# Kernel tuning notes

Measured on AMD Instinct MI355X. Metric: run time of the kernel, lower is better.

## Reference

```python
import jax, jax.numpy as jnp
import numpy as np
from jax import lax

EPS = 1e-5

def conv2d(x, w, b=None, pad=1):
    # x: [N,C,H,W], w: [O,I,kh,kw]
    out = lax.conv_general_dilated(x, w, window_strides=(1, 1),
                                   padding=[(pad, pad), (pad, pad)],
                                   dimension_numbers=('NCHW', 'OIHW', 'NCHW'))
    if b is not None:
        out = out + b[None, :, None, None]
    return out

def batchnorm(x, gamma, beta):
    # training-mode BN (biased batch stats), matching torch default train()
    mean = jnp.mean(x, axis=(0, 2, 3), keepdims=True)
    var = jnp.var(x, axis=(0, 2, 3), keepdims=True)
    xn = (x - mean) * lax.rsqrt(var + EPS)
    return xn * gamma[None, :, None, None] + beta[None, :, None, None]

def setup_inputs() -> dict:
    key = jax.random.key(0)
    ks = jax.random.split(key, 16)
    B, Cin, H, W = 4, 3, 256, 256
    Cout = 128
    NP = 32
    npat = NP // 3  # 10 per normal region
    qc_in = Cout + 3 * npat + NP  # 190 (actual concat width)

    def kaiming(k, shape, fan_in):
        return jax.random.normal(k, shape, jnp.float32) * np.sqrt(2.0 / fan_in)

    inp = {
        'x': jax.random.normal(ks[0], (B, Cin, H, W), jnp.float32),
        'conv1_w': kaiming(ks[1], (Cout // 2, Cin, 3, 3), Cin * 9),
        'conv1_b': jnp.zeros((Cout // 2,), jnp.float32),
        'bn1_g': jnp.ones((Cout // 2,), jnp.float32),
        'bn1_b': jnp.zeros((Cout // 2,), jnp.float32),
        'conv2_w': kaiming(ks[2], (Cout, Cout // 2, 3, 3), (Cout // 2) * 9),
        'conv2_b': jnp.zeros((Cout,), jnp.float32),
        'bn2_g': jnp.ones((Cout,), jnp.float32),
        'bn2_b': jnp.zeros((Cout,), jnp.float32),
        'core_p': jax.random.normal(ks[3], (npat, Cout, 3, 3), jnp.float32),
        'clad_p': jax.random.normal(ks[4], (npat, Cout, 3, 3), jnp.float32),
        'ferr_p': jax.random.normal(ks[5], (npat, Cout, 3, 3), jnp.float32),
        'anom_p': jax.random.normal(ks[6], (NP, Cout, 3, 3), jnp.float32),
        'qa1_w': kaiming(ks[7], (64, qc_in, 1, 1), qc_in),
        'qa1_b': jnp.zeros((64,), jnp.float32),
        'qa2_w': kaiming(ks[8], (1, 64, 1, 1), 64),
        'qa2_b': jnp.zeros((1,), jnp.float32),
        'cls_w': kaiming(ks[9], (4, qc_in, 1, 1), qc_in),
        'cls_b': jnp.zeros((4,), jnp.float32),
    }
    return inp

def reference(x, conv1_w, conv1_b, bn1_g, bn1_b, conv2_w, conv2_b, bn2_g, bn2_b,
              core_p, clad_p, ferr_p, anom_p, qa1_w, qa1_b, qa2_w, qa2_b, cls_w, cls_b):
    # feature extractor: conv-bn-relu x2
    h = jax.nn.relu(batchnorm(conv2d(x, conv1_w, conv1_b), bn1_g, bn1_b))
    features = jax.nn.relu(batchnorm(conv2d(h, conv2_w, conv2_b), bn2_g, bn2_b))

    # pattern matching: the per-pattern loop of 1-out-channel convs + sigmoid
    # is exactly one multi-output-channel conv (no bias) + sigmoid
    normal_w = jnp.concatenate([core_p, clad_p, ferr_p], axis=0)  # [30,C,3,3]
    all_matches = jax.nn.sigmoid(conv2d(features, normal_w))       # [B,30,H,W]
    anomaly_matches = jax.nn.sigmoid(conv2d(features, anom_p))     # [B,32,H,W]

    quality_input = jnp.concatenate([features, all_matches, anomaly_matches], axis=1)
    q = jax.nn.relu(conv2d(quality_input, qa1_w, qa1_b, pad=0))
    quality_scores = jax.nn.sigmoid(conv2d(q, qa2_w, qa2_b, pad=0))

    classifications = conv2d(quality_input, cls_w, cls_b, pad=0)
    region_logits = classifications[:, :3]
    anomaly_logits = classifications[:, 3:4]
    region_probs = jax.nn.softmax(region_logits, axis=1)
    anomaly_probs = jax.nn.sigmoid(anomaly_logits)

    return (features, region_logits, anomaly_logits, all_matches,
            anomaly_matches, quality_scores, region_probs, anomaly_probs)
```

## Files before the change

### kernel.cpp

```cpp
#include <hip/hip_runtime.h>
#include <hip/hip_bf16.h>

typedef unsigned short u16;
typedef __attribute__((ext_vector_type(8)))  short s8v;
typedef __attribute__((ext_vector_type(4)))  short s4v;
typedef __attribute__((ext_vector_type(16))) float f16v;

#define HWX 65536
#define EPSV 1e-5f

#define O0 0u
#define O1 33554432u
#define O2 34340864u
#define O3 34603008u
#define O4 42467328u
#define O5 50855936u
#define O6 51118080u
#define O7 51904512u

__device__ __forceinline__ float u2f(u16 u) {
    union { unsigned int i; float f; } v; v.i = ((unsigned int)u) << 16; return v.f;
}
__device__ __forceinline__ u16 f2u(float f) {
    __hip_bfloat16 h = __float2bfloat16(f);
    return *reinterpret_cast<u16*>(&h);
}
__device__ __forceinline__ s8v ld8(const u16* p) {
    union { s8v v; s4v h[2]; } r;
    r.h[0] = *(const s4v*)p;
    r.h[1] = *(const s4v*)(p + 4);
    return r.v;
}

#define PHYS(i) ((i) + ((i) >> 5))

__global__ __launch_bounds__(256) void k_conv1(const float* __restrict__ x,
                                               const float* __restrict__ w,
                                               const float* __restrict__ bias,
                                               u16* __restrict__ out,
                                               float* __restrict__ ssum,
                                               float* __restrict__ sqsum) {
    const int h = blockIdx.x, cb = blockIdx.y, b = blockIdx.z;
    const int t = threadIdx.x;
    const int pg = t & 31, cg = t >> 5;
    const int px0 = pg * 8, c0 = cg * 4;
    const int cbase = cb * 32;

    __shared__ float xs[3][3][266];
    __shared__ float wl[27 * 33];

    float acc[4][8];
    #pragma unroll
    for (int c = 0; c < 4; c++) {
        float bv = bias[cbase + c0 + c];
        #pragma unroll
        for (int p = 0; p < 8; p++) acc[c][p] = bv;
    }

    for (int idx = t; idx < 3 * 768; idx += 256) {
        int ci = idx / 768, rem = idx - ci * 768;
        int r = rem >> 8, px = rem & 255;
        int hh = h + r - 1;
        float v = 0.f;
        if ((unsigned)hh < 256u)
            v = x[((size_t)(b * 3 + ci) * 256 + hh) * 256 + px];
        xs[ci][r][PHYS(1 + px)] = v;
    }
    if (t < 18) {
        int ci = t / 6, rr = t - ci * 6;
        xs[ci][rr >> 1][(rr & 1) ? PHYS(257) : 0] = 0.f;
    }
    for (int idx = t; idx < 27 * 32; idx += 256) {
        int co = idx / 27, rem = idx - co * 27;
        wl[rem * 33 + co] = w[(cbase + co) * 27 + rem];
    }
    __syncthreads();

    for (int ci = 0; ci < 3; ci++) {
        #pragma unroll
        for (int kh = 0; kh < 3; kh++) {
            float xv[10];
            #pragma unroll
            for (int j = 0; j < 10; j++) xv[j] = xs[ci][kh][PHYS(px0 + j)];
            float wv[3][4];
            #pragma unroll
            for (int kw = 0; kw < 3; kw++)
                #pragma unroll
                for (int c = 0; c < 4; c++)
                    wv[kw][c] = wl[(ci * 9 + kh * 3 + kw) * 33 + c0 + c];
            #pragma unroll
            for (int c = 0; c < 4; c++)
                #pragma unroll
                for (int p = 0; p < 8; p++)
                    acc[c][p] += xv[p] * wv[0][c] + xv[p + 1] * wv[1][c]
                               + xv[p + 2] * wv[2][c];
        }
    }

    #pragma unroll
    for (int c = 0; c < 4; c++) {
        int cm = cbase + c0 + c;
        u16* op = out + (((size_t)(b * 64 + cm) * 256 + h) * 256 + px0);
        #pragma unroll
        for (int p = 0; p < 8; p++) op[p] = f2u(acc[c][p]);
    }

    __syncthreads();
    float* red = &xs[0][0][0];
    #pragma unroll
    for (int c = 0; c < 4; c++) {
        float sv = 0.f, qv = 0.f;
        #pragma unroll
        for (int p = 0; p < 8; p++) { sv += acc[c][p]; qv += acc[c][p] * acc[c][p]; }
        red[(c0 + c) * 33 + pg] = sv;
        red[1056 + (c0 + c) * 33 + pg] = qv;
    }
    __syncthreads();
    if (t < 64) {
        int co = t & 31, v = t >> 5;
        const float* base = red + v * 1056 + co * 33;
        float sum = 0.f;
        #pragma unroll
        for (int i = 0; i < 32; i++) sum += base[i];
        atomicAdd((v ? sqsum : ssum) + cbase + co, sum);
    }
}

__global__ void k_finalize(const float* __restrict__ s, const float* __restrict__ q,
                           const float* __restrict__ g, const float* __restrict__ be,
                           float* __restrict__ sc, float* __restrict__ sh, int C) {
    int c = threadIdx.x;
    if (c >= C) return;
    const float invN = 1.f / 262144.f;
    float m = s[c] * invN;
    float v = fmaxf(q[c] * invN - m * m, 0.f);
    float scale = g[c] * rsqrtf(v + EPSV);
    sc[c] = scale;
    sh[c] = be[c] - m * scale;
}

__global__ __launch_bounds__(256) void k_bnrelu_h(ushort4* __restrict__ buf,
                                                  const float* __restrict__ sc,
                                                  const float* __restrict__ sh) {
    size_t i = (size_t)blockIdx.x * 256 + threadIdx.x;
    int c = (int)(i >> 14) & 63;
    float s = sc[c], h0 = sh[c];
    ushort4 r = buf[i];
    ushort4 o;
    o.x = f2u(fmaxf(u2f(r.x) * s + h0, 0.f));
    o.y = f2u(fmaxf(u2f(r.y) * s + h0, 0.f));
    o.z = f2u(fmaxf(u2f(r.z) * s + h0, 0.f));
    o.w = f2u(fmaxf(u2f(r.w) * s + h0, 0.f));
    buf[i] = o;
}

__global__ __launch_bounds__(256) void k_bnrelu(float4* __restrict__ buf,
                                                const float* __restrict__ sc,
                                                const float* __restrict__ sh, int C) {
    size_t i = (size_t)blockIdx.x * 256 + threadIdx.x;
    int c = (int)(i >> 14) % C;
    float s = sc[c], h0 = sh[c];
    float4 r = buf[i];
    float4 o;
    o.x = fmaxf(r.x * s + h0, 0.f);
    o.y = fmaxf(r.y * s + h0, 0.f);
    o.z = fmaxf(r.z * s + h0, 0.f);
    o.w = fmaxf(r.w * s + h0, 0.f);
    buf[i] = o;
}

__global__ __launch_bounds__(256) void k_stats(const float* __restrict__ raw,
                                               float* __restrict__ ssum,
                                               float* __restrict__ sqsum) {
    const int co = blockIdx.x, seg = blockIdx.y;
    const int t = threadIdx.x;
    __shared__ float red[8];
    float s = 0.f, q = 0.f;
    for (int b = 0; b < 4; b++) {
        const float4* p = (const float4*)(raw + ((size_t)(b * 128 + co) * HWX) + seg * 8192);
        for (int i = t; i < 2048; i += 256) {
            float4 v = p[i];
            s += v.x + v.y + v.z + v.w;
            q += v.x * v.x + v.y * v.y + v.z * v.z + v.w * v.w;
        }
    }
    #pragma unroll
    for (int off = 32; off; off >>= 1) {
        s += __shfl_down(s, off, 64);
        q += __shfl_down(q, off, 64);
    }
    int lane = t & 63, wv = t >> 6;
    if (lane == 0) { red[wv] = s; red[4 + wv] = q; }
    __syncthreads();
    if (t == 0) atomicAdd(&ssum[co], red[0] + red[1] + red[2] + red[3]);
    else if (t == 1) atomicAdd(&sqsum[co], red[4] + red[5] + red[6] + red[7]);
}

__global__ void k_prep_w(const float* __restrict__ wcat, u16* __restrict__ wtile) {
    int i = blockIdx.x * 256 + threadIdx.x;
    if (i >= 159744) return;
    int ch = i / 19968, rem = i - ch * 19968;
    int pl = rem / 9984; rem -= pl * 9984;
    int kwco = rem / 52, k = rem - kwco * 52;
    int kw = kwco >> 6, co = kwco & 63;
    u16 v = 0;
    if (k < 48 && co < 62) {
        int kh = k >> 4, ci = ch * 16 + (k & 15);
        float f = wcat[(size_t)co * 1152 + ci * 9 + kh * 3 + kw];
        u16 hv = f2u(f);
        v = pl ? f2u(f - u2f(hv)) : hv;
    }
    wtile[i] = v;
}
__global__ void k_prep_w2(const float* __restrict__ w2, u16* __restrict__ wtile2) {
    int i = blockIdx.x * 256 + threadIdx.x;
    if (i >= 79872) return;
    int ch = i / 19968, rem = i - ch * 19968;
    int kwco = rem / 52, k = rem - kwco * 52;
    int kw = kwco >> 7, co = kwco & 127;
    u16 v = 0;
    if (k < 48) {
        int kh = k >> 4, ci = ch * 16 + (k & 15);
        v = f2u(w2[((size_t)co * 64 + ci) * 9 + kh * 3 + kw]);
    }
    wtile2[i] = v;
}

__device__ __forceinline__ void load_x_c2(const u16* __restrict__ hb, int b, int ch,
                                          int h, int t, unsigned xp[24]) {
    #pragma unroll
    for (int r = 0; r < 3; r++) {
        int hh = h + r - 1;
        bool vr = (unsigned)hh < 256u;
        if (vr) {
            const u16* base = hb + ((size_t)(b * 64 + ch * 16) << 16)
                            + ((size_t)hh << 8) + t;
            #pragma unroll
            for (int ci = 0; ci < 16; ci += 2) {
                unsigned a = base[(size_t)ci << 16];
                unsigned c = base[(size_t)(ci + 1) << 16];
                xp[(r * 16 + ci) >> 1] = a | (c << 16);
            }
        } else {
            #pragma unroll
            for (int ci = 0; ci < 16; ci += 2) xp[(r * 16 + ci) >> 1] = 0u;
        }
    }
}

__device__ __forceinline__ void load_x_match(const float* __restrict__ feat, int b, int ch,
                                             int h, int t, float xv[48]) {
    #pragma unroll
    for (int r = 0; r < 3; r++) {
        int hh = h + r - 1;
        bool vr = (unsigned)hh < 256u;
        if (vr) {
            const float* base = feat + ((size_t)(b * 128 + ch * 16) << 16)
                              + ((size_t)hh << 8) + t;
            #pragma unroll
            for (int ci = 0; ci < 16; ci++)
                xv[r * 16 + ci] = base[(size_t)ci << 16];
        } else {
            #pragma unroll
            for (int ci = 0; ci < 16; ci++) xv[r * 16 + ci] = 0.f;
        }
    }
}

__global__ __launch_bounds__(256, 2) void k_conv2_mf(
    const u16* __restrict__ hb, const u16* __restrict__ wtile2,
    const float* __restrict__ bias, float* __restrict__ out)
{
    const int h = blockIdx.x, b = blockIdx.y;
    const int t = threadIdx.x, l = t & 63, wv = t >> 6;
    const int kg = (l >> 5) * 8, nn = l & 31;

    __shared__ __align__(16) u16 xs[258 * 52];
    __shared__ __align__(16) u16 wl[3 * 128 * 52];

    f16v acc[2][4];
    #pragma unroll
    for (int pt = 0; pt < 2; pt++)
        #pragma unroll
        for (int s = 0; s < 4; s++)
            #pragma unroll
            for (int r = 0; r < 16; r++) acc[pt][s][r] = 0.f;

    for (int i = t; i < 258 * 52 / 4; i += 256)
        ((ushort4*)xs)[i] = ushort4{0, 0, 0, 0};
    __syncthreads();

    unsigned xp[24];
    load_x_c2(hb, b, 0, h, t, xp);

    for (int ch = 0; ch < 4; ch++) {
        {
            const int4* src = (const int4*)(wtile2 + (size_t)ch * 19968);
            for (int i = t; i < 2496; i += 256) ((int4*)wl)[i] = src[i];
        }
        #pragma unroll
        for (int r = 0; r < 3; r++) {
            if ((unsigned)(h + r - 1) < 256u) {
                #pragma unroll
                for (int g = 0; g < 4; g++) {
                    int i0 = r * 16 + g * 4;
                    uint2 hp;
                    hp.x = xp[i0 >> 1];
                    hp.y = xp[(i0 >> 1) + 1];
                    *(uint2*)&xs[(size_t)(t + 1) * 52 + i0] = hp;
                }
            }
        }
        __syncthreads();
        if (ch < 3) load_x_c2(hb, b, ch + 1, h, t, xp);
        #pragma unroll
        for (int kw = 0; kw < 3; kw++) {
            #pragma unroll
            for (int ks = 0; ks < 3; ks++) {
                int k0 = ks * 16 + kg;
                s8v af[4], bf[2];
                #pragma unroll
                for (int s = 0; s < 4; s++)
                    af[s] = ld8(&wl[(kw * 128 + s * 32 + nn) * 52 + k0]);
                #pragma unroll
                for (int pt = 0; pt < 2; pt++)
                    bf[pt] = ld8(&xs[((wv * 2 + pt) * 32 + nn + kw) * 52 + k0]);
                #pragma unroll
                for (int pt = 0; pt < 2; pt++)
                    #pragma unroll
                    for (int s = 0; s < 4; s++)
                        acc[pt][s] = __builtin_amdgcn_mfma_f32_32x32x16_bf16(
                            af[s], bf[pt], acc[pt][s], 0, 0, 0);
            }
        }
        __syncthreads();
    }

    #pragma unroll
    for (int pt = 0; pt < 2; pt++) {
        int px = (wv * 2 + pt) * 32 + nn;
        #pragma unroll
        for (int s = 0; s < 4; s++) {
            #pragma unroll
            for (int r = 0; r < 16; r++) {
                int co = s * 32 + (r & 3) + 8 * (r >> 2) + 4 * (l >> 5);
                out[(((size_t)b * 128 + co) * 256 + h) * 256 + px] = acc[pt][s][r] + bias[co];
            }
        }
    }
}

__global__ __launch_bounds__(256, 2) void k_match_mf(
    const float* __restrict__ feat, const u16* __restrict__ wtile,
    float* __restrict__ out_all, float* __restrict__ out_anom)
{
    const int h = blockIdx.x, b = blockIdx.y;
    const int t = threadIdx.x, l = t & 63, wv = t >> 6;
    const int kg = (l >> 5) * 8, nn = l & 31;

    __shared__ __align__(16) u16 xs[258 * 52];
    __shared__ __align__(16) u16 wl[2][9984];

    f16v acc[2][2];
    #pragma unroll
    for (int pt = 0; pt < 2; pt++)
        #pragma unroll
        for (int s = 0; s < 2; s++)
            #pragma unroll
            for (int r = 0; r < 16; r++) acc[pt][s][r] = 0.f;

    for (int i = t; i < 258 * 52 / 4; i += 256)
        ((ushort4*)xs)[i] = ushort4{0, 0, 0, 0};
    __syncthreads();

    float xv[48];
    load_x_match(feat, b, 0, h, t, xv);
    unsigned lor[24];

    for (int ch = 0; ch < 8; ch++) {
        {
            const int4* src = (const int4*)(wtile + (size_t)ch * 2 * 9984);
            for (int i = t; i < 2496; i += 256) ((int4*)wl[0])[i] = src[i];
        }
        #pragma unroll
        for (int r = 0; r < 3; r++) {
            bool vr = (unsigned)(h + r - 1) < 256u;
            #pragma unroll
            for (int g = 0; g < 4; g++) {
                int i0 = r * 16 + g * 4;
                u16 h0 = f2u(xv[i0 + 0]), h1 = f2u(xv[i0 + 1]);
                u16 h2 = f2u(xv[i0 + 2]), h3 = f2u(xv[i0 + 3]);
                lor[(i0 >> 1) + 0] = (unsigned)f2u(xv[i0 + 0] - u2f(h0))
                                   | ((unsigned)f2u(xv[i0 + 1] - u2f(h1)) << 16);
                lor[(i0 >> 1) + 1] = (unsigned)f2u(xv[i0 + 2] - u2f(h2))
                                   | ((unsigned)f2u(xv[i0 + 3] - u2f(h3)) << 16);
                if (vr) {
                    uint2 hp;
                    hp.x = (unsigned)h0 | ((unsigned)h1 << 16);
                    hp.y = (unsigned)h2 | ((unsigned)h3 << 16);
                    *(uint2*)&xs[(size_t)(t + 1) * 52 + i0] = hp;
                }
            }
        }
        __syncthreads();
        if (ch < 7) load_x_match(feat, b, ch + 1, h, t, xv);
        #pragma unroll
        for (int kw = 0; kw < 3; kw++) {
            #pragma unroll
            for (int ks = 0; ks < 3; ks++) {
                int k0 = ks * 16 + kg;
                s8v xfr[2];
                #pragma unroll
                for (int pt = 0; pt < 2; pt++)
                    xfr[pt] = ld8(&xs[((wv * 2 + pt) * 32 + nn + kw) * 52 + k0]);
                s8v ah0 = ld8(&wl[0][(kw * 64 + nn) * 52 + k0]);
                s8v ah1 = ld8(&wl[0][(kw * 64 + 32 + nn) * 52 + k0]);
                s8v al0 = ld8(&wl[1][(kw * 64 + nn) * 52 + k0]);
                s8v al1 = ld8(&wl[1][(kw * 64 + 32 + nn) * 52 + k0]);
                #pragma unroll
                for (int pt = 0; pt < 2; pt++) {
                    acc[pt][0] = __builtin_amdgcn_mfma_f32_32x32x16_bf16(ah0, xfr[pt], acc[pt][0], 0, 0, 0);
                    acc[pt][0] = __builtin_amdgcn_mfma_f32_32x32x16_bf16(al0, xfr[pt], acc[pt][0], 0, 0, 0);
                    acc[pt][1] = __builtin_amdgcn_mfma_f32_32x32x16_bf16(ah1, xfr[pt], acc[pt][1], 0, 0, 0);
                    acc[pt][1] = __builtin_amdgcn_mfma_f32_32x32x16_bf16(al1, xfr[pt], acc[pt][1], 0, 0, 0);
                }
            }
        }
        __syncthreads();
        #pragma unroll
        for (int r = 0; r < 3; r++) {
            if ((unsigned)(h + r - 1) < 256u) {
                #pragma unroll
                for (int g = 0; g < 4; g++) {
                    int i0 = r * 16 + g * 4;
                    uint2 lp;
                    lp.x = lor[i0 >> 1];
                    lp.y = lor[(i0 >> 1) + 1];
                    *(uint2*)&xs[(size_t)(t + 1) * 52 + i0] = lp;
                }
            }
        }
        __syncthreads();
        #pragma unroll
        for (int kw = 0; kw < 3; kw++) {
            #pragma unroll
            for (int ks = 0; ks < 3; ks++) {
                int k0 = ks * 16 + kg;
                s8v xfr[2];
                #pragma unroll
                for (int pt = 0; pt < 2; pt++)
                    xfr[pt] = ld8(&xs[((wv * 2 + pt) * 32 + nn + kw) * 52 + k0]);
                s8v ah0 = ld8(&wl[0][(kw * 64 + nn) * 52 + k0]);
                s8v ah1 = ld8(&wl[0][(kw * 64 + 32 + nn) * 52 + k0]);
                #pragma unroll
                for (int pt = 0; pt < 2; pt++) {
                    acc[pt][0] = __builtin_amdgcn_mfma_f32_32x32x16_bf16(ah0, xfr[pt], acc[pt][0], 0, 0, 0);
                    acc[pt][1] = __builtin_amdgcn_mfma_f32_32x32x16_bf16(ah1, xfr[pt], acc[pt][1], 0, 0, 0);
                }
            }
        }
        __syncthreads();
    }

    #pragma unroll
    for (int pt = 0; pt < 2; pt++) {
        int px = (wv * 2 + pt) * 32 + nn;
        #pragma unroll
        for (int s = 0; s < 2; s++) {
            #pragma unroll
            for (int r = 0; r < 16; r++) {
                int cm = s * 32 + (r & 3) + 8 * (r >> 2) + 4 * (l >> 5);
                float sg = 1.f / (1.f + __expf(-acc[pt][s][r]));
                if (cm < 30)
                    out_all[(((size_t)b * 30 + cm) * 256 + h) * 256 + px] = sg;
                else if (cm < 62)
                    out_anom[(((size_t)b * 32 + cm - 30) * 256 + h) * 256 + px] = sg;
            }
        }
    }
}

__global__ __launch_bounds__(256) void k_heads(const float* __restrict__ dout,
                                               const float* __restrict__ qa1w,
                                               const float* __restrict__ qa1b,
                                               const float* __restrict__ qa2w,
                                               const float* __restrict__ qa2b,
                                               const float* __restrict__ clsw,
                                               const float* __restrict__ clsb,
                                               float* __restrict__ out) {
    __shared__ __align__(16) float lw[190 * 68];
    __shared__ float lq2[64];
    __shared__ float lb[70];
    const int t = threadIdx.x;
    for (int i = t; i < 190 * 64; i += 256) { int j = i / 190, k = i - j * 190; lw[k * 68 + j] = qa1w[i]; }
    for (int i = t; i < 190 * 4;  i += 256) { int c = i / 190, k = i - c * 190; lw[k * 68 + 64 + c] = clsw[i]; }
    if (t < 64) { lq2[t] = qa2w[t]; lb[t] = qa1b[t]; }
    if (t < 4) lb[64 + t] = clsb[t];
    if (t == 0) lb[68] = qa2b[0];
    __syncthreads();
    const int px = blockIdx.x * 256 + t;
    const int b = blockIdx.y;
    const float* feat = dout + O0 + (size_t)b * 128 * HWX + px;
    const float* amat = dout + O3 + (size_t)b * 30 * HWX + px;
    const float* anm  = dout + O4 + (size_t)b * 32 * HWX + px;
    float acc[64];
    #pragma unroll
    for (int j = 0; j < 64; j++) acc[j] = lb[j];
    float c0 = lb[64], c1 = lb[65], c2 = lb[66], c3 = lb[67];
    for (int k = 0; k < 190; k++) {
        float val;
        if (k < 128)      val = feat[(size_t)k * HWX];
        else if (k < 158) val = amat[(size_t)(k - 128) * HWX];
        else              val = anm[(size_t)(k - 158) * HWX];
        const float4* wr = (const float4*)(lw + k * 68);
        #pragma unroll
        for (int j = 0; j < 16; j++) {
            float4 wvv = wr[j];
            acc[4 * j + 0] += val * wvv.x;
            acc[4 * j + 1] += val * wvv.y;
            acc[4 * j + 2] += val * wvv.z;
            acc[4 * j + 3] += val * wvv.w;
        }
        float4 wc = wr[16];
        c0 += val * wc.x; c1 += val * wc.y; c2 += val * wc.z; c3 += val * wc.w;
    }
    float qa = lb[68];
    #pragma unroll
    for (int j = 0; j < 64; j++) qa += fmaxf(acc[j], 0.f) * lq2[j];
    float quality = 1.f / (1.f + __expf(-qa));
    float m = fmaxf(c0, fmaxf(c1, c2));
    float e0 = __expf(c0 - m), e1 = __expf(c1 - m), e2 = __expf(c2 - m);
    float inv = 1.f / (e0 + e1 + e2);
    size_t hw = (size_t)px;
    out[O1 + ((size_t)b * 3 + 0) * HWX + hw] = c0;
    out[O1 + ((size_t)b * 3 + 1) * HWX + hw] = c1;
    out[O1 + ((size_t)b * 3 + 2) * HWX + hw] = c2;
    out[O2 + (size_t)b * HWX + hw] = c3;
    out[O5 + (size_t)b * HWX + hw] = quality;
    out[O6 + ((size_t)b * 3 + 0) * HWX + hw] = e0 * inv;
    out[O6 + ((size_t)b * 3 + 1) * HWX + hw] = e1 * inv;
    out[O6 + ((size_t)b * 3 + 2) * HWX + hw] = e2 * inv;
    out[O7 + (size_t)b * HWX + hw] = 1.f / (1.f + __expf(-c3));
}

extern "C" void kernel_launch(void* const* d_in, const int* in_sizes, int n_in,
                              void* d_out, int out_size, void* d_ws, size_t ws_size,
                              hipStream_t stream) {
    (void)in_sizes; (void)n_in; (void)out_size; (void)ws_size;
    const float* x    = (const float*)d_in[0];
    const float* w1   = (const float*)d_in[1];
    const float* b1   = (const float*)d_in[2];
    const float* g1   = (const float*)d_in[3];
    const float* be1  = (const float*)d_in[4];
    const float* w2   = (const float*)d_in[5];
    const float* b2   = (const float*)d_in[6];
    const float* g2   = (const float*)d_in[7];
    const float* be2  = (const float*)d_in[8];
    const float* core = (const float*)d_in[9];
    const float* clad = (const float*)d_in[10];
    const float* ferr = (const float*)d_in[11];
    const float* anom = (const float*)d_in[12];
    const float* qa1w = (const float*)d_in[13];
    const float* qa1b = (const float*)d_in[14];
    const float* qa2w = (const float*)d_in[15];
    const float* qa2b = (const float*)d_in[16];
    const float* clsw = (const float*)d_in[17];
    const float* clsb = (const float*)d_in[18];

    char* ws = (char*)d_ws;
    float* stats = (float*)ws;
    float* s1 = stats + 0;
    float* q1 = stats + 64;
    float* s2 = stats + 128;
    float* q2 = stats + 256;
    float* sc1 = stats + 384;
    float* sh1 = stats + 448;
    float* sc2 = stats + 512;
    float* sh2 = stats + 640;
    u16*   hraw   = (u16*)(ws + 4096);
    float* wcat   = (float*)(ws + 33558528ull);
    u16*   wtile2 = (u16*)(ws + 33844224ull);
    u16*   wtile  = (u16*)(ws + 34004224ull);
    float* dout = (float*)d_out;

    hipMemsetAsync(stats, 0, 384 * sizeof(float), stream);
    hipMemcpyAsync(wcat,             core, 10 * 1152 * 4, hipMemcpyDeviceToDevice, stream);
    hipMemcpyAsync(wcat + 10 * 1152, clad, 10 * 1152 * 4, hipMemcpyDeviceToDevice, stream);
    hipMemcpyAsync(wcat + 20 * 1152, ferr, 10 * 1152 * 4, hipMemcpyDeviceToDevice, stream);
    hipMemcpyAsync(wcat + 30 * 1152, anom, 32 * 1152 * 4, hipMemcpyDeviceToDevice, stream);

    dim3 blk(256);
    k_prep_w2<<<312, blk, 0, stream>>>(w2, wtile2);
    k_prep_w<<<624, blk, 0, stream>>>(wcat, wtile);

    k_conv1<<<dim3(256, 2, 4), blk, 0, stream>>>(x, w1, b1, hraw, s1, q1);
    k_finalize<<<1, 128, 0, stream>>>(s1, q1, g1, be1, sc1, sh1, 64);
    k_bnrelu_h<<<16384, blk, 0, stream>>>((ushort4*)hraw, sc1, sh1);

    k_conv2_mf<<<dim3(256, 4), blk, 0, stream>>>(hraw, wtile2, b2, dout + O0);
    k_stats<<<dim3(128, 8), blk, 0, stream>>>(dout + O0, s2, q2);
    k_finalize<<<1, 128, 0, stream>>>(s2, q2, g2, be2, sc2, sh2, 128);
    k_bnrelu<<<32768, blk, 0, stream>>>((float4*)(dout + O0), sc2, sh2, 128);

    k_match_mf<<<dim3(256, 4), blk, 0, stream>>>(dout + O0, wtile, dout + O3, dout + O4);
    k_heads<<<dim3(256, 4), blk, 0, stream>>>(dout, qa1w, qa1b, qa2w, qa2b, clsw, clsb, dout);
}
```

Measured before the change: 735.8 us.

## Move 1x1 quality and classifier heads onto bf16x3 MFMA with split weights

Replaces the scalar FP32 per-pixel 190x68 head GEMM with a matrix-core version. Weights are pre-split into bf16 high/low planes, and activations are split the same way in LDS. Three MFMAs per tile approximate FP32 accuracy. Next-chunk activation loads are prefetched while the current chunk computes. The goal is to cut the FMA and LDS-broadcast cost of the heads kernel. In exchange it adds a small prep kernel, reuses the wcat workspace region for the split weights, and carries a slight precision risk from the bf16x3 scheme.

Result: faster. 648.5 us (-11.9%).

```diff
diff --git a/kernel.cpp b/kernel.cpp
--- a/kernel.cpp
+++ b/kernel.cpp
@@ -224,6 +224,22 @@
         v = f2u(w2[((size_t)co * 64 + ci) * 9 + kh * 3 + kw]);
     }
     wtile2[i] = v;
+}
+__global__ void k_prep_wh(const float* __restrict__ qa1w, const float* __restrict__ clsw,
+                          u16* __restrict__ whl) {
+    int i = blockIdx.x * 256 + threadIdx.x;
+    if (i >= 46080) return;
+    int ch = i / 3840, rem = i - ch * 3840;
+    int pl = rem / 1920; rem -= pl * 1920;
+    int co = rem / 20, kloc = rem - co * 20;
+    u16 v = 0;
+    int k = ch * 16 + kloc;
+    if (kloc < 16 && k < 190 && co < 68) {
+        float f = (co < 64) ? qa1w[co * 190 + k] : clsw[(co - 64) * 190 + k];
+        u16 hv = f2u(f);
+        v = pl ? f2u(f - u2f(hv)) : hv;
+    }
+    whl[i] = v;
 }
 
 __device__ __forceinline__ void load_x_c2(const u16* __restrict__ hb, int b, int ch,
@@ -480,67 +496,136 @@
     }
 }
 
-__global__ __launch_bounds__(256) void k_heads(const float* __restrict__ dout,
-                                               const float* __restrict__ qa1w,
-                                               const float* __restrict__ qa1b,
-                                               const float* __restrict__ qa2w,
-                                               const float* __restrict__ qa2b,
-                                               const float* __restrict__ clsw,
-                                               const float* __restrict__ clsb,
-                                               float* __restrict__ out) {
-    __shared__ __align__(16) float lw[190 * 68];
-    __shared__ float lq2[64];
-    __shared__ float lb[70];
-    const int t = threadIdx.x;
-    for (int i = t; i < 190 * 64; i += 256) { int j = i / 190, k = i - j * 190; lw[k * 68 + j] = qa1w[i]; }
-    for (int i = t; i < 190 * 4;  i += 256) { int c = i / 190, k = i - c * 190; lw[k * 68 + 64 + c] = clsw[i]; }
-    if (t < 64) { lq2[t] = qa2w[t]; lb[t] = qa1b[t]; }
+__device__ __forceinline__ void load_x_heads(const float* __restrict__ fb,
+                                             const float* __restrict__ ab,
+                                             const float* __restrict__ nb,
+                                             int ch, float xv[16]) {
+    #pragma unroll
+    for (int ci = 0; ci < 16; ci++) {
+        int k = ch * 16 + ci;
+        float v;
+        if (k < 128)      v = fb[(size_t)k << 16];
+        else if (k < 158) v = ab[(size_t)(k - 128) << 16];
+        else if (k < 190) v = nb[(size_t)(k - 158) << 16];
+        else              v = 0.f;
+        xv[ci] = v;
+    }
+}
+
+__global__ __launch_bounds__(256, 2) void k_heads_mf(
+    const float* __restrict__ dout, const u16* __restrict__ whl,
+    const float* __restrict__ qa1b, const float* __restrict__ qa2w,
+    const float* __restrict__ qa2b, const float* __restrict__ clsb,
+    float* __restrict__ out)
+{
+    const int h = blockIdx.x, b = blockIdx.y;
+    const int t = threadIdx.x, l = t & 63, wv = t >> 6;
+    const int kg = (l >> 5) * 8, nn = l & 31;
+
+    __shared__ __align__(16) u16 xh[256 * 20];
+    __shared__ __align__(16) u16 xl[256 * 20];
+    __shared__ __align__(16) u16 wl2[2 * 1920];
+    __shared__ float lb[69];
+    __shared__ float lw2[64];
+
+    if (t < 64) { lb[t] = qa1b[t]; lw2[t] = qa2w[t]; }
     if (t < 4) lb[64 + t] = clsb[t];
     if (t == 0) lb[68] = qa2b[0];
-    __syncthreads();
-    const int px = blockIdx.x * 256 + t;
-    const int b = blockIdx.y;
-    const float* feat = dout + O0 + (size_t)b * 128 * HWX + px;
-    const float* amat = dout + O3 + (size_t)b * 30 * HWX + px;
-    const float* anm  = dout + O4 + (size_t)b * 32 * HWX + px;
-    float acc[64];
-    #pragma unroll
-    for (int j = 0; j < 64; j++) acc[j] = lb[j];
-    float c0 = lb[64], c1 = lb[65], c2 = lb[66], c3 = lb[67];
-    for (int k = 0; k < 190; k++) {
-        float val;
-        if (k < 128)      val = feat[(size_t)k * HWX];
-        else if (k < 158) val = amat[(size_t)(k - 128) * HWX];
-        else              val = anm[(size_t)(k - 158) * HWX];
-        const float4* wr = (const float4*)(lw + k * 68);
-        #pragma unroll
-        for (int j = 0; j < 16; j++) {
-            float4 wvv = wr[j];
-            acc[4 * j + 0] += val * wvv.x;
-            acc[4 * j + 1] += val * wvv.y;
-            acc[4 * j + 2] += val * wvv.z;
-            acc[4 * j + 3] += val * wvv.w;
-        }
-        float4 wc = wr[16];
-        c0 += val * wc.x; c1 += val * wc.y; c2 += val * wc.z; c3 += val * wc.w;
-    }
-    float qa = lb[68];
-    #pragma unroll
-    for (int j = 0; j < 64; j++) qa += fmaxf(acc[j], 0.f) * lq2[j];
-    float quality = 1.f / (1.f + __expf(-qa));
-    float m = fmaxf(c0, fmaxf(c1, c2));
-    float e0 = __expf(c0 - m), e1 = __expf(c1 - m), e2 = __expf(c2 - m);
-    float inv = 1.f / (e0 + e1 + e2);
-    size_t hw = (size_t)px;
-    out[O1 + ((size_t)b * 3 + 0) * HWX + hw] = c0;
-    out[O1 + ((size_t)b * 3 + 1) * HWX + hw] = c1;
-    out[O1 + ((size_t)b * 3 + 2) * HWX + hw] = c2;
-    out[O2 + (size_t)b * HWX + hw] = c3;
-    out[O5 + (size_t)b * HWX + hw] = quality;
-    out[O6 + ((size_t)b * 3 + 0) * HWX + hw] = e0 * inv;
-    out[O6 + ((size_t)b * 3 + 1) * HWX + hw] = e1 * inv;
-    out[O6 + ((size_t)b * 3 + 2) * HWX + hw] = e2 * inv;
-    out[O7 + (size_t)b * HWX + hw] = 1.f / (1.f + __expf(-c3));
+
+    f16v acc[3][2];
+    #pragma unroll
+    for (int s = 0; s < 3; s++)
+        #pragma unroll
+        for (int pt = 0; pt < 2; pt++)
+            #pragma unroll
+            for (int r = 0; r < 16; r++) acc[s][pt][r] = 0.f;
+
+    const float* fb = dout + O0 + (((size_t)b * 128) << 16) + ((size_t)h << 8) + t;
+    const float* ab = dout + O3 + (((size_t)b * 30) << 16) + ((size_t)h << 8) + t;
+    const float* nb = dout + O4 + (((size_t)b * 32) << 16) + ((size_t)h << 8) + t;
+
+    float xv[16];
+    load_x_heads(fb, ab, nb, 0, xv);
+
+    #pragma unroll
+    for (int ch = 0; ch < 12; ch++) {
+        {
+            const int4* src = (const int4*)(whl + (size_t)ch * 3840);
+            for (int i = t; i < 480; i += 256) ((int4*)wl2)[i] = src[i];
+        }
+        #pragma unroll
+        for (int g = 0; g < 4; g++) {
+            int i0 = g * 4;
+            u16 h0 = f2u(xv[i0 + 0]), h1 = f2u(xv[i0 + 1]);
+            u16 h2 = f2u(xv[i0 + 2]), h3 = f2u(xv[i0 + 3]);
+            uint2 hp, lp;
+            hp.x = (unsigned)h0 | ((unsigned)h1 << 16);
+            hp.y = (unsigned)h2 | ((unsigned)h3 << 16);
+            lp.x = (unsigned)f2u(xv[i0 + 0] - u2f(h0))
+                 | ((unsigned)f2u(xv[i0 + 1] - u2f(h1)) << 16);
+            lp.y = (unsigned)f2u(xv[i0 + 2] - u2f(h2))
+                 | ((unsigned)f2u(xv[i0 + 3] - u2f(h3)) << 16);
+            *(uint2*)&xh[t * 20 + i0] = hp;
+            *(uint2*)&xl[t * 20 + i0] = lp;
+        }
+        __syncthreads();
+        if (ch < 11) load_x_heads(fb, ab, nb, ch + 1, xv);
+        s8v xfh[2], xfl[2];
+        #pragma unroll
+        for (int pt = 0; pt < 2; pt++) {
+            int row = (wv * 2 + pt) * 32 + nn;
+            xfh[pt] = ld8(&xh[row * 20 + kg]);
+            xfl[pt] = ld8(&xl[row * 20 + kg]);
+        }
+        #pragma unroll
+        for (int s = 0; s < 3; s++) {
+            s8v awh = ld8(&wl2[(s * 32 + nn) * 20 + kg]);
+            s8v awl = ld8(&wl2[1920 + (s * 32 + nn) * 20 + kg]);
+            #pragma unroll
+            for (int pt = 0; pt < 2; pt++) {
+                acc[s][pt] = __builtin_amdgcn_mfma_f32_32x32x16_bf16(awh, xfh[pt], acc[s][pt], 0, 0, 0);
+                acc[s][pt] = __builtin_amdgcn_mfma_f32_32x32x16_bf16(awl, xfh[pt], acc[s][pt], 0, 0, 0);
+                acc[s][pt] = __builtin_amdgcn_mfma_f32_32x32x16_bf16(awh, xfl[pt], acc[s][pt], 0, 0, 0);
+            }
+        }
+        __syncthreads();
+    }
+
+    const int hi = l >> 5;
+    #pragma unroll
+    for (int pt = 0; pt < 2; pt++) {
+        float qa_part = 0.f;
+        #pragma unroll
+        for (int m = 0; m < 2; m++)
+            #pragma unroll
+            for (int r = 0; r < 16; r++) {
+                int row = m * 32 + (r & 3) + 8 * (r >> 2) + 4 * hi;
+                float v = acc[m][pt][r] + lb[row];
+                qa_part += fmaxf(v, 0.f) * lw2[row];
+            }
+        qa_part += __shfl_xor(qa_part, 32, 64);
+        if (hi == 0) {
+            int px = (wv * 2 + pt) * 32 + nn;
+            size_t hw = (size_t)h * 256 + px;
+            float quality = 1.f / (1.f + __expf(-(qa_part + lb[68])));
+            float c0 = acc[2][pt][0] + lb[64];
+            float c1 = acc[2][pt][1] + lb[65];
+            float c2 = acc[2][pt][2] + lb[66];
+            float c3 = acc[2][pt][3] + lb[67];
+            float m0 = fmaxf(c0, fmaxf(c1, c2));
+            float e0 = __expf(c0 - m0), e1 = __expf(c1 - m0), e2 = __expf(c2 - m0);
+            float inv = 1.f / (e0 + e1 + e2);
+            out[O1 + ((size_t)b * 3 + 0) * HWX + hw] = c0;
+            out[O1 + ((size_t)b * 3 + 1) * HWX + hw] = c1;
+            out[O1 + ((size_t)b * 3 + 2) * HWX + hw] = c2;
+            out[O2 + (size_t)b * HWX + hw] = c3;
+            out[O5 + (size_t)b * HWX + hw] = quality;
+            out[O6 + ((size_t)b * 3 + 0) * HWX + hw] = e0 * inv;
+            out[O6 + ((size_t)b * 3 + 1) * HWX + hw] = e1 * inv;
+            out[O6 + ((size_t)b * 3 + 2) * HWX + hw] = e2 * inv;
+            out[O7 + (size_t)b * HWX + hw] = 1.f / (1.f + __expf(-c3));
+        }
+    }
 }
 
 extern "C" void kernel_launch(void* const* d_in, const int* in_sizes, int n_in,
@@ -581,6 +666,7 @@
     float* wcat   = (float*)(ws + 33558528ull);
     u16*   wtile2 = (u16*)(ws + 33844224ull);
     u16*   wtile  = (u16*)(ws + 34004224ull);
+    u16*   whl    = (u16*)wcat;
     float* dout = (float*)d_out;
 
     hipMemsetAsync(stats, 0, 384 * sizeof(float), stream);
@@ -592,6 +678,7 @@
     dim3 blk(256);
     k_prep_w2<<<312, blk, 0, stream>>>(w2, wtile2);
     k_prep_w<<<624, blk, 0, stream>>>(wcat, wtile);
+    k_prep_wh<<<180, blk, 0, stream>>>(qa1w, clsw, whl);
 
     k_conv1<<<dim3(256, 2, 4), blk, 0, stream>>>(x, w1, b1, hraw, s1, q1);
     k_finalize<<<1, 128, 0, stream>>>(s1, q1, g1, be1, sc1, sh1, 64);
@@ -603,5 +690,5 @@
     k_bnrelu<<<32768, blk, 0, stream>>>((float4*)(dout + O0), sc2, sh2, 128);
 
     k_match_mf<<<dim3(256, 4), blk, 0, stream>>>(dout + O0, wtile, dout + O3, dout + O4);
-    k_heads<<<dim3(256, 4), blk, 0, stream>>>(dout, qa1w, qa1b, qa2w, qa2b, clsw, clsb, dout);
-}
+    k_heads_mf<<<dim3(256, 4), blk, 0, stream>>>(dout, whl, qa1b, qa2w, qa2b, clsb, dout);
+}
```
